# Performance work log

Measured on AMD Instinct MI355X. Metric: run time of the kernel, lower is better.

The kernel has to match this reference:

```python
import jax, jax.numpy as jnp
import numpy as np

N, E, F, H, C = 50000, 800000, 128, 256, 40
BN_EPS = 1e-5


def setup_inputs() -> dict:
    key = jax.random.key(0)
    ks = jax.random.split(key, 8)
    s = 0.05
    return {
        'x': jax.random.normal(ks[0], (N, F), jnp.float32),
        'edge_index': jax.random.randint(ks[1], (2, E), 0, N),
        'eps1': jnp.zeros((), jnp.float32),
        'W1': jax.random.normal(ks[2], (F, H), jnp.float32) * s,
        'b1': jnp.zeros((H,), jnp.float32),
        'g1': jnp.ones((H,), jnp.float32),
        'be1': jnp.zeros((H,), jnp.float32),
        'W2': jax.random.normal(ks[3], (H, H), jnp.float32) * s,
        'b2': jnp.zeros((H,), jnp.float32),
        'eps2': jnp.zeros((), jnp.float32),
        'W3': jax.random.normal(ks[4], (H, H), jnp.float32) * s,
        'b3': jnp.zeros((H,), jnp.float32),
        'g2': jnp.ones((H,), jnp.float32),
        'be2': jnp.zeros((H,), jnp.float32),
        'W4': jax.random.normal(ks[5], (H, H), jnp.float32) * s,
        'b4': jnp.zeros((H,), jnp.float32),
        'g3': jnp.ones((H,), jnp.float32),
        'be3': jnp.zeros((H,), jnp.float32),
        'Wf': jax.random.normal(ks[6], (H, C), jnp.float32) * s,
        'bf': jnp.zeros((C,), jnp.float32),
    }


def _bn(h, g, b):
    # BatchNorm1d forward with batch statistics (training-mode math, biased var)
    m = jnp.mean(h, axis=0)
    v = jnp.var(h, axis=0)
    return (h - m) * jax.lax.rsqrt(v + BN_EPS) * g + b


def _gin_conv(x, edge_index, eps, Wa, ba, g, be, Wb, bb):
    # GINConv: out = mlp((1+eps)*x + sum_{(src->dst)} x[src])
    src, dst = edge_index[0], edge_index[1]
    agg = jax.ops.segment_sum(x[src], dst, num_segments=x.shape[0])  # [N, d]
    h = (1.0 + eps) * x + agg
    h = jnp.maximum(_bn(h @ Wa + ba, g, be), 0.0)  # Linear-BN-ReLU
    return h @ Wb + bb                              # Linear


def reference(x, edge_index, eps1, W1, b1, g1, be1, W2, b2,
              eps2, W3, b3, g2, be2, W4, b4, g3, be3, Wf, bf):
    h = _gin_conv(x, edge_index, eps1, W1, b1, g1, be1, W2, b2)
    h = jnp.maximum(h, 0.0)  # F.relu (dropout p=0)
    h = _gin_conv(h, edge_index, eps2, W3, b3, g2, be2, W4, b4)
    h = jnp.maximum(_bn(h, g3, be3), 0.0)  # bn2 + relu
    return h @ Wf + bf  # fc -> [N, C]
```

## Files before the change

### kernel.cpp

```cpp
#include <hip/hip_runtime.h>
#include <hip/hip_bf16.h>


#define NN 50000
#define EE 800000
#define FDIM 128
#define HDIM 256
#define CDIM 40
#define BN_EPS 1e-5f
#define CSTRIDE 136

typedef unsigned short u16;
typedef unsigned int u32;
typedef __attribute__((ext_vector_type(8))) short short8;
typedef __attribute__((ext_vector_type(4))) float f32x4;

__device__ __forceinline__ float bflo(u32 u) { return __uint_as_float(u << 16); }
__device__ __forceinline__ float bfhi(u32 u) { return __uint_as_float(u & 0xFFFF0000u); }
__device__ __forceinline__ u16 f2bf(float f) {
  __hip_bfloat16 h = __float2bfloat16(f);
  return *(u16*)&h;
}
__device__ __forceinline__ u32 pack2(float a, float b) {
  return (u32)f2bf(a) | ((u32)f2bf(b) << 16);
}

__global__ void k_hist(const int* __restrict__ ei, int* __restrict__ deg) {
  int e = blockIdx.x * 256 + threadIdx.x;
  if (e < EE) atomicAdd(&deg[ei[EE + e]], 1);
}

__global__ void k_scan_blocks(const int* __restrict__ in, int* __restrict__ partial,
                              int* __restrict__ bsums, int n) {
  __shared__ int s[256];
  int i = blockIdx.x * 256 + threadIdx.x;
  s[threadIdx.x] = (i < n) ? in[i] : 0;
  __syncthreads();
  for (int d = 1; d < 256; d <<= 1) {
    int t = (threadIdx.x >= d) ? s[threadIdx.x - d] : 0;
    __syncthreads();
    s[threadIdx.x] += t;
    __syncthreads();
  }
  if (i < n) partial[i] = s[threadIdx.x];
  if (threadIdx.x == 255) bsums[blockIdx.x] = s[255];
}

__global__ void k_scan_sums(int* __restrict__ bs, int nb) {
  __shared__ int s[256];
  s[threadIdx.x] = (threadIdx.x < nb) ? bs[threadIdx.x] : 0;
  __syncthreads();
  for (int d = 1; d < 256; d <<= 1) {
    int t = (threadIdx.x >= d) ? s[threadIdx.x - d] : 0;
    __syncthreads();
    s[threadIdx.x] += t;
    __syncthreads();
  }
  int ex = (threadIdx.x == 0) ? 0 : s[threadIdx.x - 1];
  if (threadIdx.x < nb) bs[threadIdx.x] = ex;
}

__global__ void k_scan_add(const int* __restrict__ partial, const int* __restrict__ bs,
                           int* __restrict__ rowstart, int n) {
  int i = blockIdx.x * 256 + threadIdx.x;
  if (i < n) rowstart[i + 1] = partial[i] + bs[blockIdx.x];
  if (i == 0) rowstart[0] = 0;
}

__global__ void k_copy_i32(const int* __restrict__ a, int* __restrict__ b, int n) {
  int i = blockIdx.x * 256 + threadIdx.x;
  if (i < n) b[i] = a[i];
}

__global__ void k_scatter(const int* __restrict__ ei, int* __restrict__ cursor,
                          int* __restrict__ sorted_src) {
  int e = blockIdx.x * 256 + threadIdx.x;
  if (e < EE) {
    int dst = ei[EE + e];
    int p = atomicAdd(&cursor[dst], 1);
    sorted_src[p] = ei[e];
  }
}

__global__ void k_cvt_x(const float* __restrict__ x, u16* __restrict__ xb) {
  int i = blockIdx.x * 256 + threadIdx.x;
  size_t base = (size_t)i * 4;
  if (base < (size_t)NN * FDIM) {
    float4 v = *(const float4*)&x[base];
    u32 lo = pack2(v.x, v.y), hi = pack2(v.z, v.w);
    *(uint2*)&xb[base] = make_uint2(lo, hi);
  }
}

__global__ void k_cvt_wt(const float* __restrict__ W, u16* __restrict__ Wt, int K) {
  int i = blockIdx.x * 256 + threadIdx.x;
  int k = i >> 8, n = i & 255;
  if (k < K) Wt[(size_t)n * K + k] = f2bf(W[i]);
}

template <int FEAT>
__global__ __launch_bounds__(256)
void k_agg(const u16* __restrict__ x, const int* __restrict__ rowstart,
           const int* __restrict__ sorted_src, const float* __restrict__ epsp,
           u16* __restrict__ out) {
  int node = blockIdx.x * 4 + (threadIdx.x >> 6);
  if (node >= NN) return;
  int lane = threadIdx.x & 63;
  float e1 = 1.0f + epsp[0];
  int s = rowstart[node], t = rowstart[node + 1];
  if constexpr (FEAT == 128) {
    const u32* xp = (const u32*)x;
    u32 u = xp[(size_t)node * 64 + lane];
    float a0 = bflo(u) * e1, a1 = bfhi(u) * e1;
    int p = s;
    for (; p + 3 < t; p += 4) {
      int s0 = sorted_src[p], s1 = sorted_src[p + 1];
      int s2 = sorted_src[p + 2], s3 = sorted_src[p + 3];
      u32 u0 = xp[(size_t)s0 * 64 + lane];
      u32 u1 = xp[(size_t)s1 * 64 + lane];
      u32 u2 = xp[(size_t)s2 * 64 + lane];
      u32 u3 = xp[(size_t)s3 * 64 + lane];
      a0 += (bflo(u0) + bflo(u1)) + (bflo(u2) + bflo(u3));
      a1 += (bfhi(u0) + bfhi(u1)) + (bfhi(u2) + bfhi(u3));
    }
    for (; p < t; ++p) {
      u32 u0 = xp[(size_t)sorted_src[p] * 64 + lane];
      a0 += bflo(u0); a1 += bfhi(u0);
    }
    ((u32*)out)[(size_t)node * 64 + lane] = pack2(a0, a1);
  } else {
    const uint2* xp = (const uint2*)x;
    uint2 u = xp[(size_t)node * 64 + lane];
    float a0 = bflo(u.x) * e1, a1 = bfhi(u.x) * e1;
    float a2 = bflo(u.y) * e1, a3 = bfhi(u.y) * e1;
    int p = s;
    for (; p + 3 < t; p += 4) {
      int s0 = sorted_src[p], s1 = sorted_src[p + 1];
      int s2 = sorted_src[p + 2], s3 = sorted_src[p + 3];
      uint2 u0 = xp[(size_t)s0 * 64 + lane];
      uint2 u1 = xp[(size_t)s1 * 64 + lane];
      uint2 u2 = xp[(size_t)s2 * 64 + lane];
      uint2 u3 = xp[(size_t)s3 * 64 + lane];
      a0 += (bflo(u0.x) + bflo(u1.x)) + (bflo(u2.x) + bflo(u3.x));
      a1 += (bfhi(u0.x) + bfhi(u1.x)) + (bfhi(u2.x) + bfhi(u3.x));
      a2 += (bflo(u0.y) + bflo(u1.y)) + (bflo(u2.y) + bflo(u3.y));
      a3 += (bfhi(u0.y) + bfhi(u1.y)) + (bfhi(u2.y) + bfhi(u3.y));
    }
    for (; p < t; ++p) {
      uint2 u0 = xp[(size_t)sorted_src[p] * 64 + lane];
      a0 += bflo(u0.x); a1 += bfhi(u0.x);
      a2 += bflo(u0.y); a3 += bfhi(u0.y);
    }
    ((uint2*)out)[(size_t)node * 64 + lane] = make_uint2(pack2(a0, a1), pack2(a2, a3));
  }
}

template <int K, bool TRANSFORM, bool RELU_OUT, bool COLSUMS>
__global__ __launch_bounds__(256)
void k_gemm(const u16* __restrict__ A, const u16* __restrict__ Bt,
            const float* __restrict__ bias, const float* __restrict__ ta,
            const float* __restrict__ tc, u16* __restrict__ C,
            float* __restrict__ csum, float* __restrict__ csq) {
  constexpr int NCH = K / 8;
  constexpr int NKS = K / 32;
  __shared__ u16 Bs[128 * K];
  __shared__ u16 Cs[32 * CSTRIDE];
  __shared__ float2 Tb[K];

  const int tid = threadIdx.x;
  const int lane = tid & 63;
  const int w = tid >> 6;
  const int wm = w >> 1;
  const int wn = w & 1;
  const int lr = lane & 15, lq = lane >> 4;
  const int half = blockIdx.x & 1;
  const u16* Bth = Bt + (size_t)half * 128 * K;

  for (int i = tid; i < 128 * NCH; i += 256) {
    int row = i / NCH, c = i % NCH;
    short8 v = *(const short8*)&Bth[(size_t)row * K + c * 8];
    ((short8*)Bs)[row * NCH + (c ^ (row & 7))] = v;
  }
  if constexpr (TRANSFORM) {
    for (int k = tid; k < K; k += 256) Tb[k] = make_float2(ta[k], tc[k]);
  }

  float bv[4];
#pragma unroll
  for (int ni = 0; ni < 4; ++ni) bv[ni] = bias[half * 128 + wn * 64 + ni * 16 + lr];
  float colS[4] = {}, colQ[4] = {};

  __syncthreads();

  constexpr int NTILE = (NN + 31) / 32;
  for (int rt = blockIdx.x >> 1; rt < NTILE; rt += 256) {
    int row = rt * 32 + wm * 16 + lr;
    int rowc = row < NN ? row : NN - 1;
    const u16* Ap = &A[(size_t)rowc * K];

    short8 areg[NKS];
#pragma unroll
    for (int ks = 0; ks < NKS; ++ks)
      areg[ks] = *(const short8*)&Ap[ks * 32 + lq * 8];

    if constexpr (TRANSFORM) {
#pragma unroll
      for (int ks = 0; ks < NKS; ++ks) {
        short8 v = areg[ks];
#pragma unroll
        for (int j = 0; j < 8; ++j) {
          float2 tb = Tb[ks * 32 + lq * 8 + j];
          float f = __uint_as_float(((u32)(u16)v[j]) << 16);
          v[j] = (short)f2bf(fmaxf(fmaf(f, tb.x, tb.y), 0.f));
        }
        areg[ks] = v;
      }
    }

    f32x4 acc[4];
#pragma unroll
    for (int ni = 0; ni < 4; ++ni) acc[ni] = (f32x4){0.f, 0.f, 0.f, 0.f};
#pragma unroll
    for (int ks = 0; ks < NKS; ++ks) {
#pragma unroll
      for (int ni = 0; ni < 4; ++ni) {
        int col = wn * 64 + ni * 16 + lr;
        int c = (ks * 4 + lq) ^ (col & 7);
        short8 bfr = ((const short8*)Bs)[col * NCH + c];
        acc[ni] = __builtin_amdgcn_mfma_f32_16x16x32_bf16(areg[ks], bfr, acc[ni], 0, 0, 0);
      }
    }

#pragma unroll
    for (int ni = 0; ni < 4; ++ni) {
      int col = wn * 64 + ni * 16 + lr;
#pragma unroll
      for (int j = 0; j < 4; ++j) {
        int r = wm * 16 + lq * 4 + j;
        float v = acc[ni][j] + bv[ni];
        if constexpr (RELU_OUT) v = fmaxf(v, 0.f);
        if constexpr (COLSUMS) {
          if (rt * 32 + r < NN) { colS[ni] += v; colQ[ni] += v * v; }
        }
        Cs[r * CSTRIDE + col] = f2bf(v);
      }
    }
    __syncthreads();
    {
      int r = tid >> 3;
      int gr = rt * 32 + r;
      if (gr < NN) {
        const uint4* src = (const uint4*)&Cs[r * CSTRIDE + (tid & 7) * 16];
        uint4 v0 = src[0], v1 = src[1];
        uint4* dst = (uint4*)&C[(size_t)gr * HDIM + half * 128 + (tid & 7) * 16];
        dst[0] = v0; dst[1] = v1;
      }
    }
    __syncthreads();
  }

  if constexpr (COLSUMS) {
#pragma unroll
    for (int ni = 0; ni < 4; ++ni) {
      float s = colS[ni], q = colQ[ni];
      s += __shfl_xor(s, 16); s += __shfl_xor(s, 32);
      q += __shfl_xor(q, 16); q += __shfl_xor(q, 32);
      if (lq == 0) {
        int col = half * 128 + wn * 64 + ni * 16 + lr;
        atomicAdd(&csum[col], s);
        atomicAdd(&csq[col], q);
      }
    }
  }
}

__global__ void k_bn_fin(const float* __restrict__ sum, const float* __restrict__ sq,
                         const float* __restrict__ g, const float* __restrict__ be,
                         float* __restrict__ a, float* __restrict__ c) {
  int t = threadIdx.x;
  float m = sum[t] * (1.0f / NN);
  float var = sq[t] * (1.0f / NN) - m * m;
  float s = g[t] * rsqrtf(var + BN_EPS);
  a[t] = s;
  c[t] = be[t] - m * s;
}

__global__ __launch_bounds__(256)
void k_gemm_final(const u16* __restrict__ A, const float* __restrict__ B,
                  const float* __restrict__ bias, const float* __restrict__ ta,
                  const float* __restrict__ tc, float* __restrict__ C) {
  __shared__ float As[64][65];
  __shared__ float Bs[64][CDIM];
  int tid = threadIdx.x;
  int r = tid & 63, q = tid >> 6;
  int r0 = blockIdx.x * 64;
  float acc[10] = {};
  for (int k0 = 0; k0 < HDIM; k0 += 64) {
#pragma unroll
    for (int i = 0; i < 4; ++i) {
      int idx = tid + i * 256;
      int row = idx >> 4;
      int c4 = (idx & 15) * 4;
      int gr = r0 + row;
      float v0 = 0.f, v1 = 0.f, v2 = 0.f, v3 = 0.f;
      if (gr < NN) {
        uint2 u = *(const uint2*)&A[(size_t)gr * HDIM + k0 + c4];
        v0 = fmaxf(fmaf(bflo(u.x), ta[k0 + c4 + 0], tc[k0 + c4 + 0]), 0.f);
        v1 = fmaxf(fmaf(bfhi(u.x), ta[k0 + c4 + 1], tc[k0 + c4 + 1]), 0.f);
        v2 = fmaxf(fmaf(bflo(u.y), ta[k0 + c4 + 2], tc[k0 + c4 + 2]), 0.f);
        v3 = fmaxf(fmaf(bfhi(u.y), ta[k0 + c4 + 3], tc[k0 + c4 + 3]), 0.f);
      }
      As[c4 + 0][row] = v0;
      As[c4 + 1][row] = v1;
      As[c4 + 2][row] = v2;
      As[c4 + 3][row] = v3;
    }
#pragma unroll
    for (int i = 0; i < 10; ++i) {
      int idx = tid + i * 256;
      int row = idx / CDIM;
      int col = idx % CDIM;
      Bs[row][col] = B[(size_t)(k0 + row) * CDIM + col];
    }
    __syncthreads();
#pragma unroll
    for (int k = 0; k < 64; ++k) {
      float a = As[k][r];
#pragma unroll
      for (int j = 0; j < 10; ++j) acc[j] = fmaf(a, Bs[k][q * 10 + j], acc[j]);
    }
    __syncthreads();
  }
  int gr = r0 + r;
  if (gr < NN) {
#pragma unroll
    for (int j = 0; j < 10; ++j) C[(size_t)gr * CDIM + q * 10 + j] = acc[j] + bias[q * 10 + j];
  }
}

extern "C" void kernel_launch(void* const* d_in, const int* in_sizes, int n_in,
                              void* d_out, int out_size, void* d_ws, size_t ws_size,
                              hipStream_t stream) {
  const float* x   = (const float*)d_in[0];
  const int*   ei  = (const int*)d_in[1];
  const float* eps1= (const float*)d_in[2];
  const float* W1  = (const float*)d_in[3];
  const float* b1  = (const float*)d_in[4];
  const float* g1  = (const float*)d_in[5];
  const float* be1 = (const float*)d_in[6];
  const float* W2  = (const float*)d_in[7];
  const float* b2  = (const float*)d_in[8];
  const float* eps2= (const float*)d_in[9];
  const float* W3  = (const float*)d_in[10];
  const float* b3  = (const float*)d_in[11];
  const float* g2  = (const float*)d_in[12];
  const float* be2 = (const float*)d_in[13];
  const float* W4  = (const float*)d_in[14];
  const float* b4  = (const float*)d_in[15];
  const float* g3  = (const float*)d_in[16];
  const float* be3 = (const float*)d_in[17];
  const float* Wf  = (const float*)d_in[18];
  const float* bf  = (const float*)d_in[19];
  float* out = (float*)d_out;

  char* p = (char*)d_ws;
  auto alloc = [&](size_t bytes) -> char* {
    char* r = p;
    p += (bytes + 255) & ~(size_t)255;
    return r;
  };
  float* stats   = (float*)alloc(12 * 256 * sizeof(float));
  int* deg       = (int*)alloc(NN * sizeof(int));
  int* rowstart  = (int*)alloc((NN + 16) * sizeof(int));
  int* cursor    = (int*)alloc(NN * sizeof(int));
  int* sorted    = (int*)alloc(EE * sizeof(int));
  int* partial   = (int*)alloc(NN * sizeof(int));
  int* bsums     = (int*)alloc(1024 * sizeof(int));
  u16* W1t       = (u16*)alloc(256 * 128 * sizeof(u16));
  u16* W2t       = (u16*)alloc(256 * 256 * sizeof(u16));
  u16* W3t       = (u16*)alloc(256 * 256 * sizeof(u16));
  u16* W4t       = (u16*)alloc(256 * 256 * sizeof(u16));
  u16* xb        = (u16*)alloc((size_t)NN * 128 * sizeof(u16));
  u16* A1        = (u16*)alloc((size_t)NN * 128 * sizeof(u16));
  u16* z1        = (u16*)alloc((size_t)NN * 256 * sizeof(u16));
  u16* h1        = (u16*)alloc((size_t)NN * 256 * sizeof(u16));
  u16* A2        = (u16*)alloc((size_t)NN * 256 * sizeof(u16));
  (void)alloc(64 * 1024);
  u16* z2 = z1;
  u16* z3 = h1;

  hipMemsetAsync(deg, 0, NN * sizeof(int), stream);
  hipMemsetAsync(stats, 0, 12 * 256 * sizeof(float), stream);

  const int nbE = (EE + 255) / 256;
  const int nbN = (NN + 255) / 256;

  k_hist<<<nbE, 256, 0, stream>>>(ei, deg);
  k_scan_blocks<<<nbN, 256, 0, stream>>>(deg, partial, bsums, NN);
  k_scan_sums<<<1, 256, 0, stream>>>(bsums, nbN);
  k_scan_add<<<nbN, 256, 0, stream>>>(partial, bsums, rowstart, NN);
  k_copy_i32<<<nbN, 256, 0, stream>>>(rowstart, cursor, NN);
  k_scatter<<<nbE, 256, 0, stream>>>(ei, cursor, sorted);

  k_cvt_x<<<(NN * FDIM / 4 + 255) / 256, 256, 0, stream>>>(x, xb);
  k_cvt_wt<<<128, 256, 0, stream>>>(W1, W1t, 128);
  k_cvt_wt<<<256, 256, 0, stream>>>(W2, W2t, 256);
  k_cvt_wt<<<256, 256, 0, stream>>>(W3, W3t, 256);
  k_cvt_wt<<<256, 256, 0, stream>>>(W4, W4t, 256);

  k_agg<128><<<(NN + 3) / 4, 256, 0, stream>>>(xb, rowstart, sorted, eps1, A1);
  k_gemm<128, false, false, true><<<512, 256, 0, stream>>>(
      A1, W1t, b1, nullptr, nullptr, z1, stats + 0, stats + 256);
  k_bn_fin<<<1, 256, 0, stream>>>(stats + 0, stats + 256, g1, be1,
                                  stats + 2 * 256, stats + 3 * 256);
  k_gemm<256, true, true, false><<<512, 256, 0, stream>>>(
      z1, W2t, b2, stats + 2 * 256, stats + 3 * 256, h1, nullptr, nullptr);

  k_agg<256><<<(NN + 3) / 4, 256, 0, stream>>>(h1, rowstart, sorted, eps2, A2);
  k_gemm<256, false, false, true><<<512, 256, 0, stream>>>(
      A2, W3t, b3, nullptr, nullptr, z2, stats + 4 * 256, stats + 5 * 256);
  k_bn_fin<<<1, 256, 0, stream>>>(stats + 4 * 256, stats + 5 * 256, g2, be2,
                                  stats + 6 * 256, stats + 7 * 256);
  k_gemm<256, true, false, true><<<512, 256, 0, stream>>>(
      z2, W4t, b4, stats + 6 * 256, stats + 7 * 256, z3, stats + 8 * 256, stats + 9 * 256);
  k_bn_fin<<<1, 256, 0, stream>>>(stats + 8 * 256, stats + 9 * 256, g3, be3,
                                  stats + 10 * 256, stats + 11 * 256);

  k_gemm_final<<<(NN + 63) / 64, 256, 0, stream>>>(
      z3, Wf, bf, stats + 10 * 256, stats + 11 * 256, out);
}
```

Before: 397.0 us.

## Double-buffer GEMM A-tile loads and widen aggregation gather unroll to 8

The GEMM kernel now prefetches the next row tile's A fragments into a second register buffer while the current tile's MFMAs run, ping-ponging between two buffers, and raises wave priority around the MFMA loop. The aggregation kernel issues eight independent neighbor gathers per iteration instead of four, with a 2-wide and single tail. These aim to hide global-load latency in both kernels, at the cost of more live registers, which could lower occupancy.

```diff
diff --git a/kernel.cpp b/kernel.cpp
--- a/kernel.cpp
+++ b/kernel.cpp
@@ -113,17 +113,20 @@
     u32 u = xp[(size_t)node * 64 + lane];
     float a0 = bflo(u) * e1, a1 = bfhi(u) * e1;
     int p = s;
-    for (; p + 3 < t; p += 4) {
-      int s0 = sorted_src[p], s1 = sorted_src[p + 1];
-      int s2 = sorted_src[p + 2], s3 = sorted_src[p + 3];
-      u32 u0 = xp[(size_t)s0 * 64 + lane];
-      u32 u1 = xp[(size_t)s1 * 64 + lane];
-      u32 u2 = xp[(size_t)s2 * 64 + lane];
-      u32 u3 = xp[(size_t)s3 * 64 + lane];
-      a0 += (bflo(u0) + bflo(u1)) + (bflo(u2) + bflo(u3));
-      a1 += (bfhi(u0) + bfhi(u1)) + (bfhi(u2) + bfhi(u3));
-    }
-    for (; p < t; ++p) {
+    for (; p + 7 < t; p += 8) {
+      u32 uu[8];
+#pragma unroll
+      for (int i = 0; i < 8; ++i) uu[i] = xp[(size_t)sorted_src[p + i] * 64 + lane];
+#pragma unroll
+      for (int i = 0; i < 8; ++i) { a0 += bflo(uu[i]); a1 += bfhi(uu[i]); }
+    }
+    for (; p + 1 < t; p += 2) {
+      u32 u0 = xp[(size_t)sorted_src[p] * 64 + lane];
+      u32 u1 = xp[(size_t)sorted_src[p + 1] * 64 + lane];
+      a0 += bflo(u0) + bflo(u1);
+      a1 += bfhi(u0) + bfhi(u1);
+    }
+    if (p < t) {
       u32 u0 = xp[(size_t)sorted_src[p] * 64 + lane];
       a0 += bflo(u0); a1 += bfhi(u0);
     }
@@ -134,19 +137,25 @@
     float a0 = bflo(u.x) * e1, a1 = bfhi(u.x) * e1;
     float a2 = bflo(u.y) * e1, a3 = bfhi(u.y) * e1;
     int p = s;
-    for (; p + 3 < t; p += 4) {
-      int s0 = sorted_src[p], s1 = sorted_src[p + 1];
-      int s2 = sorted_src[p + 2], s3 = sorted_src[p + 3];
-      uint2 u0 = xp[(size_t)s0 * 64 + lane];
-      uint2 u1 = xp[(size_t)s1 * 64 + lane];
-      uint2 u2 = xp[(size_t)s2 * 64 + lane];
-      uint2 u3 = xp[(size_t)s3 * 64 + lane];
-      a0 += (bflo(u0.x) + bflo(u1.x)) + (bflo(u2.x) + bflo(u3.x));
-      a1 += (bfhi(u0.x) + bfhi(u1.x)) + (bfhi(u2.x) + bfhi(u3.x));
-      a2 += (bflo(u0.y) + bflo(u1.y)) + (bflo(u2.y) + bflo(u3.y));
-      a3 += (bfhi(u0.y) + bfhi(u1.y)) + (bfhi(u2.y) + bfhi(u3.y));
-    }
-    for (; p < t; ++p) {
+    for (; p + 7 < t; p += 8) {
+      uint2 uu[8];
+#pragma unroll
+      for (int i = 0; i < 8; ++i) uu[i] = xp[(size_t)sorted_src[p + i] * 64 + lane];
+#pragma unroll
+      for (int i = 0; i < 8; ++i) {
+        a0 += bflo(uu[i].x); a1 += bfhi(uu[i].x);
+        a2 += bflo(uu[i].y); a3 += bfhi(uu[i].y);
+      }
+    }
+    for (; p + 1 < t; p += 2) {
+      uint2 u0 = xp[(size_t)sorted_src[p] * 64 + lane];
+      uint2 u1 = xp[(size_t)sorted_src[p + 1] * 64 + lane];
+      a0 += bflo(u0.x) + bflo(u1.x);
+      a1 += bfhi(u0.x) + bfhi(u1.x);
+      a2 += bflo(u0.y) + bflo(u1.y);
+      a3 += bfhi(u0.y) + bfhi(u1.y);
+    }
+    if (p < t) {
       uint2 u0 = xp[(size_t)sorted_src[p] * 64 + lane];
       a0 += bflo(u0.x); a1 += bfhi(u0.x);
       a2 += bflo(u0.y); a3 += bfhi(u0.y);
@@ -163,6 +172,7 @@
             float* __restrict__ csum, float* __restrict__ csq) {
   constexpr int NCH = K / 8;
   constexpr int NKS = K / 32;
+  constexpr int NTILE = (NN + 31) / 32;
   __shared__ u16 Bs[128 * K];
   __shared__ u16 Cs[32 * CSTRIDE];
   __shared__ float2 Tb[K];
@@ -170,8 +180,7 @@
   const int tid = threadIdx.x;
   const int lane = tid & 63;
   const int w = tid >> 6;
-  const int wm = w >> 1;
-  const int wn = w & 1;
+  const int wm = w >> 1, wn = w & 1;
   const int lr = lane & 15, lq = lane >> 4;
   const int half = blockIdx.x & 1;
   const u16* Bth = Bt + (size_t)half * 128 * K;
@@ -192,34 +201,37 @@
 
   __syncthreads();
 
-  constexpr int NTILE = (NN + 31) / 32;
-  for (int rt = blockIdx.x >> 1; rt < NTILE; rt += 256) {
+  short8 bufA[NKS], bufB[NKS];
+
+  auto LOADA = [&](short8* dst, int rt) {
     int row = rt * 32 + wm * 16 + lr;
     int rowc = row < NN ? row : NN - 1;
     const u16* Ap = &A[(size_t)rowc * K];
-
-    short8 areg[NKS];
 #pragma unroll
     for (int ks = 0; ks < NKS; ++ks)
-      areg[ks] = *(const short8*)&Ap[ks * 32 + lq * 8];
-
+      dst[ks] = *(const short8*)&Ap[ks * 32 + lq * 8];
+  };
+
+  auto BODY = [&](short8* cur, short8* nxt, int rt) {
     if constexpr (TRANSFORM) {
 #pragma unroll
       for (int ks = 0; ks < NKS; ++ks) {
-        short8 v = areg[ks];
+        short8 v = cur[ks];
 #pragma unroll
         for (int j = 0; j < 8; ++j) {
           float2 tb = Tb[ks * 32 + lq * 8 + j];
           float f = __uint_as_float(((u32)(u16)v[j]) << 16);
           v[j] = (short)f2bf(fmaxf(fmaf(f, tb.x, tb.y), 0.f));
         }
-        areg[ks] = v;
-      }
-    }
+        cur[ks] = v;
+      }
+    }
+    if (rt + 256 < NTILE) LOADA(nxt, rt + 256);
 
     f32x4 acc[4];
 #pragma unroll
     for (int ni = 0; ni < 4; ++ni) acc[ni] = (f32x4){0.f, 0.f, 0.f, 0.f};
+    __builtin_amdgcn_s_setprio(1);
 #pragma unroll
     for (int ks = 0; ks < NKS; ++ks) {
 #pragma unroll
@@ -227,9 +239,10 @@
         int col = wn * 64 + ni * 16 + lr;
         int c = (ks * 4 + lq) ^ (col & 7);
         short8 bfr = ((const short8*)Bs)[col * NCH + c];
-        acc[ni] = __builtin_amdgcn_mfma_f32_16x16x32_bf16(areg[ks], bfr, acc[ni], 0, 0, 0);
-      }
-    }
+        acc[ni] = __builtin_amdgcn_mfma_f32_16x16x32_bf16(cur[ks], bfr, acc[ni], 0, 0, 0);
+      }
+    }
+    __builtin_amdgcn_s_setprio(0);
 
 #pragma unroll
     for (int ni = 0; ni < 4; ++ni) {
@@ -257,6 +270,12 @@
       }
     }
     __syncthreads();
+  };
+
+  LOADA(bufA, blockIdx.x >> 1);
+  for (int rt = blockIdx.x >> 1; rt < NTILE; rt += 512) {
+    BODY(bufA, bufB, rt);
+    if (rt + 256 < NTILE) BODY(bufB, bufA, rt + 256);
   }
 
   if constexpr (COLSUMS) {
```

After: 391.4 us. Within noise of the previous version (-1.4%).
